# Kernel tuning notes

Measured on AMD Instinct MI355X. Metric: run time of the kernel, lower is better.

Reference implementation:

```python
import jax, jax.numpy as jnp
import numpy as np
import math

N_HEAD = 16
MEM_LEN = 512


def setup_inputs() -> dict:
    key = jax.random.key(0)
    ks = jax.random.split(key, 4)
    B, T, C = 4, 2048, 1024
    x = jax.random.normal(ks[0], (B, T, C), dtype=jnp.float32)
    W_attn = jax.random.normal(ks[1], (C, 3 * C), dtype=jnp.float32) * (1.0 / math.sqrt(C))
    b_attn = jnp.zeros((3 * C,), dtype=jnp.float32)
    W_proj = jax.random.normal(ks[2], (C, C), dtype=jnp.float32) * (1.0 / math.sqrt(C))
    b_proj = jnp.zeros((C,), dtype=jnp.float32)
    return {"x": x, "W_attn": W_attn, "b_attn": b_attn, "W_proj": W_proj, "b_proj": b_proj}


def reference(x, W_attn, b_attn, W_proj, b_proj):
    B, T, C = x.shape
    H = N_HEAD
    Dh = C // H
    # fused qkv projection (torch Linear with weight stored as [in, out])
    qkv = x @ W_attn + b_attn                      # [B, T, 3C]
    q, k, v = jnp.split(qkv, 3, axis=-1)
    q = q.reshape(B, T, H, Dh).transpose(0, 2, 1, 3)  # [B, H, T, Dh]
    k = k.reshape(B, T, H, Dh).transpose(0, 2, 1, 3)
    v = v.reshape(B, T, H, Dh).transpose(0, 2, 1, 3)
    # manual attention: QK^T, causal mask, softmax, att @ V
    att = jnp.einsum('bhtd,bhsd->bhts', q, k) * (1.0 / math.sqrt(Dh))  # [B,H,T,T]
    causal = jnp.tril(jnp.ones((T, T), dtype=bool))
    att = jnp.where(causal[None, None, :, :], att, jnp.finfo(att.dtype).min)
    att = jax.nn.softmax(att, axis=-1)
    y = jnp.einsum('bhts,bhsd->bhtd', att, v)      # [B, H, T, Dh]
    y = y.transpose(0, 2, 1, 3).reshape(B, T, C)
    out = y @ W_proj + b_proj                      # resid_dropout is identity (p=0 / eval)
    new_memory = x[:, -MEM_LEN:, :]
    return out, new_memory
```

## Files before the change

kernel.cpp:

```cpp
#include <hip/hip_runtime.h>
#include <hip/hip_bf16.h>

typedef __bf16 bf16;
typedef __bf16 bf16x8 __attribute__((ext_vector_type(8)));
typedef __bf16 bf16x4v __attribute__((ext_vector_type(4)));
typedef float f32x4 __attribute__((ext_vector_type(4)));
typedef float f32x16 __attribute__((ext_vector_type(16)));
typedef float float4v __attribute__((ext_vector_type(4)));
typedef unsigned int uint32x4 __attribute__((ext_vector_type(4)));

#define MFMA16(a, b, c) __builtin_amdgcn_mfma_f32_16x16x32_bf16(a, b, c, 0, 0, 0)
#define MFMA32(a, b, c) __builtin_amdgcn_mfma_f32_32x32x16_bf16(a, b, c, 0, 0, 0)

#define SCALE_Q 0.1803368801111f

__device__ __forceinline__ void async_load16(const bf16* g, bf16* l) {
    __builtin_amdgcn_global_load_lds(
        (const __attribute__((address_space(1))) void*)g,
        (__attribute__((address_space(3))) void*)l,
        16, 0, 0);
}

__device__ __forceinline__ unsigned int pack2bf(float a, float b) {
    bf16 x = (bf16)a, y = (bf16)b;
    unsigned short ux = __builtin_bit_cast(unsigned short, x);
    unsigned short uy = __builtin_bit_cast(unsigned short, y);
    return (unsigned int)ux | ((unsigned int)uy << 16);
}


__global__ void k_pre(const float* __restrict__ x, const float* __restrict__ W_attn,
                      const float* __restrict__ W_proj,
                      bf16* __restrict__ xpk, float* __restrict__ out_mem,
                      bf16* __restrict__ Wapk, bf16* __restrict__ Wppk) {
    int bid = blockIdx.x, tid = threadIdx.x;
    int lane = tid & 63;
    if (bid < 4096) {
        int line = bid * 4 + (tid >> 6);
        int slab = line >> 5, kc = line & 31;
        int t = slab * 16 + (lane & 15);
        int k = kc * 32 + (lane >> 4) * 8;
        const float* src = x + (size_t)t * 1024 + k;
        float4v v0 = *(const float4v*)src;
        float4v v1 = *(const float4v*)(src + 4);
        bf16x8 o;
        o[0] = (bf16)v0.x; o[1] = (bf16)v0.y; o[2] = (bf16)v0.z; o[3] = (bf16)v0.w;
        o[4] = (bf16)v1.x; o[5] = (bf16)v1.y; o[6] = (bf16)v1.z; o[7] = (bf16)v1.w;
        *(bf16x8*)(xpk + (size_t)line * 512 + lane * 8) = o;
        int tb = t & 2047;
        if (tb >= 1536) {
            float* dst = out_mem + ((size_t)(t >> 11) * 512 + (tb - 1536)) * 1024 + k;
            *(float4v*)dst = v0;
            *(float4v*)(dst + 4) = v1;
        }
    } else if (bid < 4096 + 1536) {
        int line = (bid - 4096) * 4 + (tid >> 6);
        int slab = line >> 5, kc = line & 31;
        int n = slab * 16 + (lane & 15);
        int k = kc * 32 + (lane >> 4) * 8;
        bf16x8 o;
#pragma unroll
        for (int j = 0; j < 8; ++j)
            o[j] = (bf16)W_attn[(size_t)(k + j) * 3072 + n];
        *(bf16x8*)(Wapk + (size_t)line * 512 + lane * 8) = o;
    } else {
        int line = (bid - 5632) * 4 + (tid >> 6);
        int slab = line >> 5, kc = line & 31;
        int n = slab * 16 + (lane & 15);
        int k = kc * 32 + (lane >> 4) * 8;
        bf16x8 o;
#pragma unroll
        for (int j = 0; j < 8; ++j)
            o[j] = (bf16)W_proj[(size_t)(k + j) * 1024 + n];
        *(bf16x8*)(Wppk + (size_t)line * 512 + lane * 8) = o;
    }
}

#define GEMM_NOLDS_BODY84                                                                \
    const bf16* Abase = Apk + (size_t)(((row0 >> 4) + wr * 8) * 32) * 512 + lane * 8;    \
    const bf16* Bbase = Bpk + (size_t)(((col0 >> 4) + wc * 4) * 32) * 512 + lane * 8;    \
    f32x4 acc[8][4] = {};                                                                \
    bf16x8 a0[8], b0[4], a1[8], b1[4];                                                   \
    _Pragma("unroll")                                                                    \
    for (int m = 0; m < 8; ++m) a0[m] = *(const bf16x8*)(Abase + m * 16384);             \
    _Pragma("unroll")                                                                    \
    for (int n = 0; n < 4; ++n) b0[n] = *(const bf16x8*)(Bbase + n * 16384);             \
    for (int t = 0; t < 16; ++t) {                                                       \
        int o1 = (2 * t + 1) * 512;                                                      \
        _Pragma("unroll")                                                                \
        for (int m = 0; m < 8; ++m) a1[m] = *(const bf16x8*)(Abase + m * 16384 + o1);    \
        _Pragma("unroll")                                                                \
        for (int n = 0; n < 4; ++n) b1[n] = *(const bf16x8*)(Bbase + n * 16384 + o1);    \
        __builtin_amdgcn_s_setprio(1);                                                   \
        _Pragma("unroll")                                                                \
        for (int m = 0; m < 8; ++m)                                                      \
            _Pragma("unroll")                                                            \
            for (int n = 0; n < 4; ++n)                                                  \
                acc[m][n] = MFMA16(a0[m], b0[n], acc[m][n]);                             \
        __builtin_amdgcn_s_setprio(0);                                                   \
        if (t < 15) {                                                                    \
            int o2 = (2 * t + 2) * 512;                                                  \
            _Pragma("unroll")                                                            \
            for (int m = 0; m < 8; ++m) a0[m] = *(const bf16x8*)(Abase + m * 16384 + o2);\
            _Pragma("unroll")                                                            \
            for (int n = 0; n < 4; ++n) b0[n] = *(const bf16x8*)(Bbase + n * 16384 + o2);\
        }                                                                                \
        __builtin_amdgcn_s_setprio(1);                                                   \
        _Pragma("unroll")                                                                \
        for (int m = 0; m < 8; ++m)                                                      \
            _Pragma("unroll")                                                            \
            for (int n = 0; n < 4; ++n)                                                  \
                acc[m][n] = MFMA16(a1[m], b1[n], acc[m][n]);                             \
        __builtin_amdgcn_s_setprio(0);                                                   \
    }

__global__ __launch_bounds__(256, 2) void k_gemm_qkv(
    const bf16* __restrict__ Apk, const bf16* __restrict__ Bpk,
    const float* __restrict__ bias,
    bf16* __restrict__ qo, bf16* __restrict__ ko, bf16* __restrict__ vo) {
    int orig = blockIdx.x;
    int wg = (orig & 7) * 96 + (orig >> 3);
    int row0 = (wg / 24) * 256;
    int col0 = (wg % 24) * 128;
    int lane = threadIdx.x & 63, w = threadIdx.x >> 6;
    int wr = w >> 1, wc = w & 1;
    int lrow = lane & 15, lks = lane >> 4;

    GEMM_NOLDS_BODY84

    int trowb = row0 + wr * 128 + lks * 4;
    int tcolb = col0 + wc * 64 + lrow;
#pragma unroll
    for (int mf = 0; mf < 8; ++mf)
#pragma unroll
        for (int nf = 0; nf < 4; ++nf) {
            int cg = tcolb + nf * 16;
            float bi = bias[cg];
#pragma unroll
            for (int j2 = 0; j2 < 4; ++j2) {
                int rg = trowb + mf * 16 + j2;
                float val = acc[mf][nf][j2] + bi;
                int b = rg >> 11, tt = rg & 2047;
                if (cg < 1024) {
                    int h = cg >> 6, d = cg & 63;
                    size_t base = (size_t)(b * 16 + h) * 131072;
                    size_t idx = base + (size_t)((((tt >> 5) * 4 + (d >> 4)) * 64 + ((d >> 3) & 1) * 32 + (tt & 31)) * 8 + (d & 7));
                    qo[idx] = (bf16)(val * SCALE_Q);
                } else if (cg < 2048) {
                    int c2 = cg - 1024;
                    int h = c2 >> 6, d = c2 & 63;
                    size_t base = (size_t)(b * 16 + h) * 131072;
                    size_t idx = base + (size_t)((((tt >> 5) * 4 + (d >> 4)) * 64 + ((d >> 3) & 1) * 32 + (tt & 31)) * 8 + (d & 7));
                    ko[idx] = (bf16)val;
                } else {
                    int c2 = cg - 2048;
                    int h = c2 >> 6, d = c2 & 63;
                    size_t base = (size_t)(b * 16 + h) * 131072;
                    size_t idx = base + (size_t)(((((tt >> 6) * 4 + ((tt >> 4) & 3)) * 2 + (d >> 5)) * 64 + ((tt >> 3) & 1) * 32 + (d & 31)) * 8 + (tt & 7));
                    vo[idx] = (bf16)val;
                }
            }
        }
}

__global__ __launch_bounds__(256, 2) void k_gemm_proj(
    const bf16* __restrict__ Apk, const bf16* __restrict__ Bpk,
    const float* __restrict__ bias, float* __restrict__ out) {
    int orig = blockIdx.x;
    int wg = (orig & 7) * 32 + (orig >> 3);
    int row0 = (wg >> 3) * 256;
    int col0 = (wg & 7) * 128;
    int lane = threadIdx.x & 63, w = threadIdx.x >> 6;
    int wr = w >> 1, wc = w & 1;
    int lrow = lane & 15, lks = lane >> 4;

    GEMM_NOLDS_BODY84

    int trowb = row0 + wr * 128 + lks * 4;
    int tcolb = col0 + wc * 64 + lrow;
#pragma unroll
    for (int mf = 0; mf < 8; ++mf)
#pragma unroll
        for (int nf = 0; nf < 4; ++nf) {
            int cg = tcolb + nf * 16;
            float bi = bias[cg];
#pragma unroll
            for (int j2 = 0; j2 < 4; ++j2) {
                int rg = trowb + mf * 16 + j2;
                out[(size_t)rg * 1024 + cg] = acc[mf][nf][j2] + bi;
            }
        }
}

__global__ __launch_bounds__(256, 2) void k_attn(
    const bf16* __restrict__ qp, const bf16* __restrict__ kp,
    const bf16* __restrict__ vp, bf16* __restrict__ ypk) {
    __shared__ __align__(16) bf16 Ks[2][4096];
    __shared__ __align__(16) bf16 Vs[2][4096];
    int id = blockIdx.x;
    int bxp = (id >> 3) & 7;
    int bh = (id & 7) + 8 * (id >> 6);
    int b = bh >> 4;
    int lane = threadIdx.x & 63, w = threadIdx.x >> 6;
    int tl = lane & 31, hi = lane >> 5;
    int lane8 = lane * 8;
    const bf16* Qb = qp + (size_t)bh * 131072;
    const bf16* Kb = kp + (size_t)bh * 131072;
    const bf16* Vb = vp + (size_t)bh * 131072;

    for (int qpass = 0; qpass < 2; ++qpass) {
        int qt0 = (qpass ? 15 - bxp : bxp) * 128;
        int trow0 = qt0 + w * 32;
        int t_g = trow0 + tl;

        bf16x8 qf[4];
        int qs = (trow0 >> 5) * 4;
#pragma unroll
        for (int kc = 0; kc < 4; ++kc)
            qf[kc] = *(const bf16x8*)&Qb[(qs + kc) * 512 + lane8];

        f32x16 o[2] = {};
        float m = -1e30f, l = 0.f;
        int ntb = (qt0 >> 6) + 2;
        int cur = 0;

#pragma unroll
        for (int i = 0; i < 2; ++i) {
            int u = 2 * w + i;
            async_load16(Kb + (size_t)u * 512 + lane8, &Ks[0][u * 512]);
            async_load16(Vb + (size_t)u * 512 + lane8, &Vs[0][u * 512]);
        }

        for (int ti = 0; ti < ntb; ++ti) {
            int s0 = ti * 64;
            if (ti + 1 < ntb) {
#pragma unroll
                for (int i = 0; i < 2; ++i) {
                    int u = 2 * w + i;
                    async_load16(Kb + (size_t)((ti + 1) * 8 + u) * 512 + lane8, &Ks[cur ^ 1][u * 512]);
                    async_load16(Vb + (size_t)((ti + 1) * 8 + u) * 512 + lane8, &Vs[cur ^ 1][u * 512]);
                }
                asm volatile("s_waitcnt vmcnt(4)" ::: "memory");
            } else {
                asm volatile("s_waitcnt vmcnt(0)" ::: "memory");
            }
            __builtin_amdgcn_sched_barrier(0);
            __builtin_amdgcn_s_barrier();
            __builtin_amdgcn_sched_barrier(0);

            if (s0 < trow0 + 32) {
                f32x16 accs[2] = {};
                __builtin_amdgcn_s_setprio(1);
#pragma unroll
                for (int st = 0; st < 2; ++st)
#pragma unroll
                    for (int kc = 0; kc < 4; ++kc) {
                        bf16x8 kf = *(const bf16x8*)&Ks[cur][(st * 4 + kc) * 512 + lane8];
                        accs[st] = MFMA32(kf, qf[kc], accs[st]);
                    }
                __builtin_amdgcn_s_setprio(0);

                if (s0 + 63 > trow0) {
#pragma unroll
                    for (int st = 0; st < 2; ++st)
#pragma unroll
                        for (int r = 0; r < 16; ++r) {
                            int s = s0 + st * 32 + (r & 3) + 8 * (r >> 2) + 4 * hi;
                            if (s > t_g) accs[st][r] = -1e30f;
                        }
                }
                float pmax = -1e30f;
#pragma unroll
                for (int st = 0; st < 2; ++st)
#pragma unroll
                    for (int r = 0; r < 16; ++r)
                        pmax = fmaxf(pmax, accs[st][r]);
                pmax = fmaxf(pmax, __shfl_xor(pmax, 32));
                if (!__all(pmax <= m + 8.0f)) {
                    float mn = fmaxf(m, pmax);
                    float corr = __builtin_amdgcn_exp2f(m - mn);
                    m = mn;
                    l *= corr;
#pragma unroll
                    for (int dt = 0; dt < 2; ++dt)
#pragma unroll
                        for (int r = 0; r < 16; ++r)
                            o[dt][r] *= corr;
                }
                float ls = 0.f;
#pragma unroll
                for (int st = 0; st < 2; ++st)
#pragma unroll
                    for (int r = 0; r < 16; ++r) {
                        float p = __builtin_amdgcn_exp2f(accs[st][r] - m);
                        accs[st][r] = p;
                        ls += p;
                    }
                ls += __shfl_xor(ls, 32);
                l += ls;

                unsigned int pk[16];
#pragma unroll
                for (int st = 0; st < 2; ++st)
#pragma unroll
                    for (int q = 0; q < 8; ++q)
                        pk[st * 8 + q] = pack2bf(accs[st][2 * q], accs[st][2 * q + 1]);
                unsigned int rv[8];
#pragma unroll
                for (int st = 0; st < 2; ++st)
#pragma unroll
                    for (int i = 0; i < 4; ++i) {
                        int base = st * 8 + (i < 2 ? i : i + 2);
                        unsigned int send = hi ? pk[base] : pk[base + 2];
                        rv[st * 4 + i] = __shfl_xor(send, 32);
                    }
                __builtin_amdgcn_s_setprio(1);
#pragma unroll
                for (int c = 0; c < 4; ++c) {
                    const int st = c >> 1, c2 = c & 1;
                    uint32x4 pw;
                    pw.x = hi ? rv[st * 4 + 2 * c2]     : pk[st * 8 + 4 * c2];
                    pw.y = hi ? rv[st * 4 + 2 * c2 + 1] : pk[st * 8 + 4 * c2 + 1];
                    pw.z = hi ? pk[st * 8 + 4 * c2 + 2] : rv[st * 4 + 2 * c2];
                    pw.w = hi ? pk[st * 8 + 4 * c2 + 3] : rv[st * 4 + 2 * c2 + 1];
                    bf16x8 pf = __builtin_bit_cast(bf16x8, pw);
#pragma unroll
                    for (int dt = 0; dt < 2; ++dt) {
                        bf16x8 vf = *(const bf16x8*)&Vs[cur][(c * 2 + dt) * 512 + lane8];
                        o[dt] = MFMA32(vf, pf, o[dt]);
                    }
                }
                __builtin_amdgcn_s_setprio(0);
            }
            asm volatile("s_waitcnt lgkmcnt(0)" ::: "memory");
            __builtin_amdgcn_sched_barrier(0);
            __builtin_amdgcn_s_barrier();
            __builtin_amdgcn_sched_barrier(0);
            cur ^= 1;
        }

        int grow = b * 2048 + t_g;
        int slab = grow >> 4;
        int hkc = (bh & 15) * 2;
        float inv = 1.0f / l;
#pragma unroll
        for (int dt = 0; dt < 2; ++dt)
#pragma unroll
            for (int rq = 0; rq < 4; ++rq) {
                bf16x4v ov;
#pragma unroll
                for (int ri = 0; ri < 4; ++ri)
                    ov[ri] = (bf16)(o[dt][rq * 4 + ri] * inv);
                size_t idx = (size_t)(slab * 32 + hkc + dt) * 512 + rq * 128 + (grow & 15) * 8 + 4 * hi;
                *(bf16x4v*)&ypk[idx] = ov;
            }
    }
}

extern "C" void kernel_launch(void* const* d_in, const int* in_sizes, int n_in,
                              void* d_out, int out_size, void* d_ws, size_t ws_size,
                              hipStream_t stream) {
    const float* x = (const float*)d_in[0];
    const float* W_attn = (const float*)d_in[1];
    const float* b_attn = (const float*)d_in[2];
    const float* W_proj = (const float*)d_in[3];
    const float* b_proj = (const float*)d_in[4];
    float* out = (float*)d_out;
    float* out_mem = out + (size_t)8388608;

    char* ws = (char*)d_ws;
    bf16* xpk  = (bf16*)(ws);
    bf16* Wapk = (bf16*)(ws + ((size_t)16 << 20));
    bf16* Wppk = (bf16*)(ws + ((size_t)22 << 20));
    bf16* q    = (bf16*)(ws + ((size_t)24 << 20));
    bf16* k    = (bf16*)(ws + ((size_t)40 << 20));
    bf16* vT   = (bf16*)(ws + ((size_t)56 << 20));
    bf16* ypk  = (bf16*)(ws + ((size_t)72 << 20));

    k_pre<<<6144, 256, 0, stream>>>(x, W_attn, W_proj, xpk, out_mem, Wapk, Wppk);
    k_gemm_qkv<<<768, 256, 0, stream>>>(xpk, Wapk, b_attn, q, k, vT);
    k_attn<<<512, 256, 0, stream>>>(q, k, vT, ypk);
    k_gemm_proj<<<256, 256, 0, stream>>>(ypk, Wppk, b_proj, out);
}
```

Baseline: 165.4 us.

## Split attention into one block per query tile with balanced causal ordering

The attention kernel no longer loops over two paired query tiles (light plus heavy) inside one block. It launches 1024 blocks, each handling a single 128-row query tile, with a remapped block index that keeps heads on the same XCD and interleaves short and long causal tiles across dispatch waves. Launch bounds are raised to 4 blocks per CU so more blocks can be resident at once and hide latency. The tradeoff is losing the built-in per-block load balance of the paired tiles, relying on dispatch order instead, plus possible register pressure from the tighter occupancy target.

```diff
diff --git a/kernel.cpp b/kernel.cpp
--- a/kernel.cpp
+++ b/kernel.cpp
@@ -192,14 +192,17 @@
         }
 }
 
-__global__ __launch_bounds__(256, 2) void k_attn(
+__global__ __launch_bounds__(256, 4) void k_attn(
     const bf16* __restrict__ qp, const bf16* __restrict__ kp,
     const bf16* __restrict__ vp, bf16* __restrict__ ypk) {
     __shared__ __align__(16) bf16 Ks[2][4096];
     __shared__ __align__(16) bf16 Vs[2][4096];
     int id = blockIdx.x;
-    int bxp = (id >> 3) & 7;
-    int bh = (id & 7) + 8 * (id >> 6);
+    int c = id & 255, r = id >> 8;
+    int xcd = c & 7, u = c >> 3;
+    int bh = xcd + 8 * (u >> 2);
+    int j = (u & 3) * 4 + r;
+    int bxp = (j & 1) ? 15 - (j >> 1) : (j >> 1);
     int b = bh >> 4;
     int lane = threadIdx.x & 63, w = threadIdx.x >> 6;
     int tl = lane & 31, hi = lane >> 5;
@@ -208,153 +211,151 @@
     const bf16* Kb = kp + (size_t)bh * 131072;
     const bf16* Vb = vp + (size_t)bh * 131072;
 
-    for (int qpass = 0; qpass < 2; ++qpass) {
-        int qt0 = (qpass ? 15 - bxp : bxp) * 128;
-        int trow0 = qt0 + w * 32;
-        int t_g = trow0 + tl;
-
-        bf16x8 qf[4];
-        int qs = (trow0 >> 5) * 4;
-#pragma unroll
-        for (int kc = 0; kc < 4; ++kc)
-            qf[kc] = *(const bf16x8*)&Qb[(qs + kc) * 512 + lane8];
-
-        f32x16 o[2] = {};
-        float m = -1e30f, l = 0.f;
-        int ntb = (qt0 >> 6) + 2;
-        int cur = 0;
-
-#pragma unroll
-        for (int i = 0; i < 2; ++i) {
-            int u = 2 * w + i;
-            async_load16(Kb + (size_t)u * 512 + lane8, &Ks[0][u * 512]);
-            async_load16(Vb + (size_t)u * 512 + lane8, &Vs[0][u * 512]);
-        }
-
-        for (int ti = 0; ti < ntb; ++ti) {
-            int s0 = ti * 64;
-            if (ti + 1 < ntb) {
-#pragma unroll
-                for (int i = 0; i < 2; ++i) {
-                    int u = 2 * w + i;
-                    async_load16(Kb + (size_t)((ti + 1) * 8 + u) * 512 + lane8, &Ks[cur ^ 1][u * 512]);
-                    async_load16(Vb + (size_t)((ti + 1) * 8 + u) * 512 + lane8, &Vs[cur ^ 1][u * 512]);
-                }
-                asm volatile("s_waitcnt vmcnt(4)" ::: "memory");
-            } else {
-                asm volatile("s_waitcnt vmcnt(0)" ::: "memory");
-            }
-            __builtin_amdgcn_sched_barrier(0);
-            __builtin_amdgcn_s_barrier();
-            __builtin_amdgcn_sched_barrier(0);
-
-            if (s0 < trow0 + 32) {
-                f32x16 accs[2] = {};
-                __builtin_amdgcn_s_setprio(1);
+    int qt0 = bxp * 128;
+    int trow0 = qt0 + w * 32;
+    int t_g = trow0 + tl;
+
+    bf16x8 qf[4];
+    int qs = (trow0 >> 5) * 4;
+#pragma unroll
+    for (int kc = 0; kc < 4; ++kc)
+        qf[kc] = *(const bf16x8*)&Qb[(qs + kc) * 512 + lane8];
+
+    f32x16 o[2] = {};
+    float m = -1e30f, l = 0.f;
+    int ntb = (qt0 >> 6) + 2;
+    int cur = 0;
+
+#pragma unroll
+    for (int i = 0; i < 2; ++i) {
+        int u2 = 2 * w + i;
+        async_load16(Kb + (size_t)u2 * 512 + lane8, &Ks[0][u2 * 512]);
+        async_load16(Vb + (size_t)u2 * 512 + lane8, &Vs[0][u2 * 512]);
+    }
+
+    for (int ti = 0; ti < ntb; ++ti) {
+        int s0 = ti * 64;
+        if (ti + 1 < ntb) {
+#pragma unroll
+            for (int i = 0; i < 2; ++i) {
+                int u2 = 2 * w + i;
+                async_load16(Kb + (size_t)((ti + 1) * 8 + u2) * 512 + lane8, &Ks[cur ^ 1][u2 * 512]);
+                async_load16(Vb + (size_t)((ti + 1) * 8 + u2) * 512 + lane8, &Vs[cur ^ 1][u2 * 512]);
+            }
+            asm volatile("s_waitcnt vmcnt(4)" ::: "memory");
+        } else {
+            asm volatile("s_waitcnt vmcnt(0)" ::: "memory");
+        }
+        __builtin_amdgcn_sched_barrier(0);
+        __builtin_amdgcn_s_barrier();
+        __builtin_amdgcn_sched_barrier(0);
+
+        if (s0 < trow0 + 32) {
+            f32x16 accs[2] = {};
+            __builtin_amdgcn_s_setprio(1);
+#pragma unroll
+            for (int st = 0; st < 2; ++st)
+#pragma unroll
+                for (int kc = 0; kc < 4; ++kc) {
+                    bf16x8 kf = *(const bf16x8*)&Ks[cur][(st * 4 + kc) * 512 + lane8];
+                    accs[st] = MFMA32(kf, qf[kc], accs[st]);
+                }
+            __builtin_amdgcn_s_setprio(0);
+
+            if (s0 + 63 > trow0) {
 #pragma unroll
                 for (int st = 0; st < 2; ++st)
 #pragma unroll
-                    for (int kc = 0; kc < 4; ++kc) {
-                        bf16x8 kf = *(const bf16x8*)&Ks[cur][(st * 4 + kc) * 512 + lane8];
-                        accs[st] = MFMA32(kf, qf[kc], accs[st]);
+                    for (int rr = 0; rr < 16; ++rr) {
+                        int s = s0 + st * 32 + (rr & 3) + 8 * (rr >> 2) + 4 * hi;
+                        if (s > t_g) accs[st][rr] = -1e30f;
                     }
-                __builtin_amdgcn_s_setprio(0);
-
-                if (s0 + 63 > trow0) {
-#pragma unroll
-                    for (int st = 0; st < 2; ++st)
-#pragma unroll
-                        for (int r = 0; r < 16; ++r) {
-                            int s = s0 + st * 32 + (r & 3) + 8 * (r >> 2) + 4 * hi;
-                            if (s > t_g) accs[st][r] = -1e30f;
-                        }
-                }
-                float pmax = -1e30f;
-#pragma unroll
-                for (int st = 0; st < 2; ++st)
-#pragma unroll
-                    for (int r = 0; r < 16; ++r)
-                        pmax = fmaxf(pmax, accs[st][r]);
-                pmax = fmaxf(pmax, __shfl_xor(pmax, 32));
-                if (!__all(pmax <= m + 8.0f)) {
-                    float mn = fmaxf(m, pmax);
-                    float corr = __builtin_amdgcn_exp2f(m - mn);
-                    m = mn;
-                    l *= corr;
-#pragma unroll
-                    for (int dt = 0; dt < 2; ++dt)
-#pragma unroll
-                        for (int r = 0; r < 16; ++r)
-                            o[dt][r] *= corr;
-                }
-                float ls = 0.f;
-#pragma unroll
-                for (int st = 0; st < 2; ++st)
-#pragma unroll
-                    for (int r = 0; r < 16; ++r) {
-                        float p = __builtin_amdgcn_exp2f(accs[st][r] - m);
-                        accs[st][r] = p;
-                        ls += p;
-                    }
-                ls += __shfl_xor(ls, 32);
-                l += ls;
-
-                unsigned int pk[16];
-#pragma unroll
-                for (int st = 0; st < 2; ++st)
-#pragma unroll
-                    for (int q = 0; q < 8; ++q)
-                        pk[st * 8 + q] = pack2bf(accs[st][2 * q], accs[st][2 * q + 1]);
-                unsigned int rv[8];
-#pragma unroll
-                for (int st = 0; st < 2; ++st)
-#pragma unroll
-                    for (int i = 0; i < 4; ++i) {
-                        int base = st * 8 + (i < 2 ? i : i + 2);
-                        unsigned int send = hi ? pk[base] : pk[base + 2];
-                        rv[st * 4 + i] = __shfl_xor(send, 32);
-                    }
-                __builtin_amdgcn_s_setprio(1);
-#pragma unroll
-                for (int c = 0; c < 4; ++c) {
-                    const int st = c >> 1, c2 = c & 1;
-                    uint32x4 pw;
-                    pw.x = hi ? rv[st * 4 + 2 * c2]     : pk[st * 8 + 4 * c2];
-                    pw.y = hi ? rv[st * 4 + 2 * c2 + 1] : pk[st * 8 + 4 * c2 + 1];
-                    pw.z = hi ? pk[st * 8 + 4 * c2 + 2] : rv[st * 4 + 2 * c2];
-                    pw.w = hi ? pk[st * 8 + 4 * c2 + 3] : rv[st * 4 + 2 * c2 + 1];
-                    bf16x8 pf = __builtin_bit_cast(bf16x8, pw);
-#pragma unroll
-                    for (int dt = 0; dt < 2; ++dt) {
-                        bf16x8 vf = *(const bf16x8*)&Vs[cur][(c * 2 + dt) * 512 + lane8];
-                        o[dt] = MFMA32(vf, pf, o[dt]);
-                    }
-                }
-                __builtin_amdgcn_s_setprio(0);
-            }
-            asm volatile("s_waitcnt lgkmcnt(0)" ::: "memory");
-            __builtin_amdgcn_sched_barrier(0);
-            __builtin_amdgcn_s_barrier();
-            __builtin_amdgcn_sched_barrier(0);
-            cur ^= 1;
-        }
-
-        int grow = b * 2048 + t_g;
-        int slab = grow >> 4;
-        int hkc = (bh & 15) * 2;
-        float inv = 1.0f / l;
-#pragma unroll
-        for (int dt = 0; dt < 2; ++dt)
-#pragma unroll
-            for (int rq = 0; rq < 4; ++rq) {
-                bf16x4v ov;
-#pragma unroll
-                for (int ri = 0; ri < 4; ++ri)
-                    ov[ri] = (bf16)(o[dt][rq * 4 + ri] * inv);
-                size_t idx = (size_t)(slab * 32 + hkc + dt) * 512 + rq * 128 + (grow & 15) * 8 + 4 * hi;
-                *(bf16x4v*)&ypk[idx] = ov;
-            }
+            }
+            float pmax = -1e30f;
+#pragma unroll
+            for (int st = 0; st < 2; ++st)
+#pragma unroll
+                for (int rr = 0; rr < 16; ++rr)
+                    pmax = fmaxf(pmax, accs[st][rr]);
+            pmax = fmaxf(pmax, __shfl_xor(pmax, 32));
+            if (!__all(pmax <= m + 8.0f)) {
+                float mn = fmaxf(m, pmax);
+                float corr = __builtin_amdgcn_exp2f(m - mn);
+                m = mn;
+                l *= corr;
+#pragma unroll
+                for (int dt = 0; dt < 2; ++dt)
+#pragma unroll
+                    for (int rr = 0; rr < 16; ++rr)
+                        o[dt][rr] *= corr;
+            }
+            float ls = 0.f;
+#pragma unroll
+            for (int st = 0; st < 2; ++st)
+#pragma unroll
+                for (int rr = 0; rr < 16; ++rr) {
+                    float p = __builtin_amdgcn_exp2f(accs[st][rr] - m);
+                    accs[st][rr] = p;
+                    ls += p;
+                }
+            ls += __shfl_xor(ls, 32);
+            l += ls;
+
+            unsigned int pk[16];
+#pragma unroll
+            for (int st = 0; st < 2; ++st)
+#pragma unroll
+                for (int q = 0; q < 8; ++q)
+                    pk[st * 8 + q] = pack2bf(accs[st][2 * q], accs[st][2 * q + 1]);
+            unsigned int rv[8];
+#pragma unroll
+            for (int st = 0; st < 2; ++st)
+#pragma unroll
+                for (int i = 0; i < 4; ++i) {
+                    int base = st * 8 + (i < 2 ? i : i + 2);
+                    unsigned int send = hi ? pk[base] : pk[base + 2];
+                    rv[st * 4 + i] = __shfl_xor(send, 32);
+                }
+            __builtin_amdgcn_s_setprio(1);
+#pragma unroll
+            for (int cc = 0; cc < 4; ++cc) {
+                const int st = cc >> 1, c2 = cc & 1;
+                uint32x4 pw;
+                pw.x = hi ? rv[st * 4 + 2 * c2]     : pk[st * 8 + 4 * c2];
+                pw.y = hi ? rv[st * 4 + 2 * c2 + 1] : pk[st * 8 + 4 * c2 + 1];
+                pw.z = hi ? pk[st * 8 + 4 * c2 + 2] : rv[st * 4 + 2 * c2];
+                pw.w = hi ? pk[st * 8 + 4 * c2 + 3] : rv[st * 4 + 2 * c2 + 1];
+                bf16x8 pf = __builtin_bit_cast(bf16x8, pw);
+#pragma unroll
+                for (int dt = 0; dt < 2; ++dt) {
+                    bf16x8 vf = *(const bf16x8*)&Vs[cur][(cc * 2 + dt) * 512 + lane8];
+                    o[dt] = MFMA32(vf, pf, o[dt]);
+                }
+            }
+            __builtin_amdgcn_s_setprio(0);
+        }
+        asm volatile("s_waitcnt lgkmcnt(0)" ::: "memory");
+        __builtin_amdgcn_sched_barrier(0);
+        __builtin_amdgcn_s_barrier();
+        __builtin_amdgcn_sched_barrier(0);
+        cur ^= 1;
     }
+
+    int grow = b * 2048 + t_g;
+    int slab = grow >> 4;
+    int hkc = (bh & 15) * 2;
+    float inv = 1.0f / l;
+#pragma unroll
+    for (int dt = 0; dt < 2; ++dt)
+#pragma unroll
+        for (int rq = 0; rq < 4; ++rq) {
+            bf16x4v ov;
+#pragma unroll
+            for (int ri = 0; ri < 4; ++ri)
+                ov[ri] = (bf16)(o[dt][rq * 4 + ri] * inv);
+            size_t idx = (size_t)(slab * 32 + hkc + dt) * 512 + rq * 128 + (grow & 15) * 8 + 4 * hi;
+            *(bf16x4v*)&ypk[idx] = ov;
+        }
 }
 
 extern "C" void kernel_launch(void* const* d_in, const int* in_sizes, int n_in,
@@ -379,6 +380,6 @@
 
     k_pre<<<6144, 256, 0, stream>>>(x, W_attn, W_proj, xpk, out_mem, Wapk, Wppk);
     k_gemm_qkv<<<768, 256, 0, stream>>>(xpk, Wapk, b_attn, q, k, vT);
-    k_attn<<<512, 256, 0, stream>>>(q, k, vT, ypk);
+    k_attn<<<1024, 256, 0, stream>>>(q, k, vT, ypk);
     k_gemm_proj<<<256, 256, 0, stream>>>(ypk, Wppk, b_proj, out);
 }
```

Result: no change. 162.7 us (-1.6%).
